# Kernel tuning notes

Hardware: AMD Instinct MI355X
Metric: run time of the kernel (lower is better)

## Reference

```python
import jax, jax.numpy as jnp
import numpy as np

N = 16384   # points (batch=1, divisible by patch_size so padding is identity)
C = 512     # channels
H = 8       # num_heads
K = 1024    # patch_size
G = 48      # voxel grid extent
EPS = 1e-5
SCALE = (C // H) ** -0.5


def setup_inputs() -> dict:
    rng = np.random.default_rng(0)
    # unique occupied voxels
    flat = rng.choice(G ** 3, size=N, replace=False)
    gx = flat // (G * G); gy = (flat // G) % G; gz = flat % G
    coords = np.stack([gx, gy, gz], 1).astype(np.int64)
    # occupancy LUT on padded grid -> neighbor index per 3x3x3 kernel offset (-1 = empty)
    lut = -np.ones(((G + 2) ** 3,), np.int64)
    def flt(c):
        return ((c[:, 0] + 1) * (G + 2) + (c[:, 1] + 1)) * (G + 2) + (c[:, 2] + 1)
    lut[flt(coords)] = np.arange(N)
    offs = np.array([[dx, dy, dz] for dx in (-1, 0, 1) for dy in (-1, 0, 1) for dz in (-1, 0, 1)], np.int64)
    nbr = np.stack([lut[flt(coords + o)] for o in offs], 1)  # [N,27]
    # Morton (z-order) serialization order
    def spread(v):
        v = v.astype(np.int64); r = np.zeros_like(v)
        for b in range(6):
            r |= ((v >> b) & 1) << (3 * b)
        return r
    code = (spread(gx) << 2) | (spread(gy) << 1) | spread(gz)
    order = np.argsort(code, kind='stable').astype(np.int32)

    key = jax.random.key(0)
    ks = jax.random.split(key, 8)
    s = 0.02
    p = lambda k, shape: jax.random.normal(k, shape, jnp.float32) * s
    return dict(
        feat=jax.random.normal(ks[0], (N, C), jnp.float32),
        neighbor_idx=jnp.asarray(nbr, jnp.int32),
        order=jnp.asarray(order, jnp.int32),
        cpe_w=p(ks[1], (27, C, C)), cpe_b=jnp.zeros((C,), jnp.float32),
        cpe_lin_w=p(ks[2], (C, C)), cpe_lin_b=jnp.zeros((C,), jnp.float32),
        cpe_ln_g=jnp.ones((C,), jnp.float32), cpe_ln_b=jnp.zeros((C,), jnp.float32),
        ln1_g=jnp.ones((C,), jnp.float32), ln1_b=jnp.zeros((C,), jnp.float32),
        qkv_w=p(ks[3], (3 * C, C)), qkv_b=jnp.zeros((3 * C,), jnp.float32),
        proj_w=p(ks[4], (C, C)), proj_b=jnp.zeros((C,), jnp.float32),
        ln2_g=jnp.ones((C,), jnp.float32), ln2_b=jnp.zeros((C,), jnp.float32),
        fc1_w=p(ks[5], (4 * C, C)), fc1_b=jnp.zeros((4 * C,), jnp.float32),
        fc2_w=p(ks[6], (C, 4 * C)), fc2_b=jnp.zeros((C,), jnp.float32),
    )


def _ln(x, g, b):
    m = x.mean(-1, keepdims=True)
    v = ((x - m) ** 2).mean(-1, keepdims=True)
    return (x - m) * jax.lax.rsqrt(v + EPS) * g + b


def _block(feat, neighbor_idx, order, cpe_w, cpe_b, cpe_lin_w, cpe_lin_b,
           cpe_ln_g, cpe_ln_b, ln1_g, ln1_b, qkv_w, qkv_b, proj_w, proj_b,
           ln2_g, ln2_b, fc1_w, fc1_b, fc2_w, fc2_b):
    # ---- CPE: SubMConv3d(3x3x3) -> Linear -> LayerNorm, residual ----
    valid = neighbor_idx >= 0
    idx = jnp.maximum(neighbor_idx, 0)
    h = jnp.zeros_like(feat)
    for kk in range(27):  # fixed kernel volume
        g = jnp.where(valid[:, kk:kk + 1], feat[idx[:, kk]], 0.0)
        h = h + g @ cpe_w[kk].T
    h = h + cpe_b
    h = h @ cpe_lin_w.T + cpe_lin_b
    h = _ln(h, cpe_ln_g, cpe_ln_b)
    feat = feat + h
    # ---- Serialized windowed attention (pre-norm, residual) ----
    x = _ln(feat, ln1_g, ln1_b)
    qkv = (x @ qkv_w.T + qkv_b)[order]                 # gather by serialized order
    qkv = qkv.reshape(N // K, K, 3, H, C // H)         # [P,K,3,H,hd]
    q = qkv[:, :, 0].transpose(0, 2, 1, 3)             # [P,H,K,hd]
    k = qkv[:, :, 1].transpose(0, 2, 1, 3)
    v = qkv[:, :, 2].transpose(0, 2, 1, 3)
    attn = jax.nn.softmax(jnp.einsum('phkd,phjd->phkj', q * SCALE, k), axis=-1)
    o = jnp.einsum('phkj,phjd->phkd', attn, v).transpose(0, 2, 1, 3).reshape(N, C)
    inverse = jnp.argsort(order)                       # scatter back
    o = o[inverse] @ proj_w.T + proj_b
    feat = feat + o
    # ---- MLP (pre-norm, residual) ----
    x = _ln(feat, ln2_g, ln2_b)
    x = jax.nn.gelu(x @ fc1_w.T + fc1_b, approximate=False)
    x = x @ fc2_w.T + fc2_b
    return feat + x


def reference(feat, neighbor_idx, order, cpe_w, cpe_b, cpe_lin_w, cpe_lin_b,
              cpe_ln_g, cpe_ln_b, ln1_g, ln1_b, qkv_w, qkv_b, proj_w, proj_b,
              ln2_g, ln2_b, fc1_w, fc1_b, fc2_w, fc2_b):
    return _block(feat, neighbor_idx, order, cpe_w, cpe_b, cpe_lin_w, cpe_lin_b,
                  cpe_ln_g, cpe_ln_b, ln1_g, ln1_b, qkv_w, qkv_b, proj_w, proj_b,
                  ln2_g, ln2_b, fc1_w, fc1_b, fc2_w, fc2_b)
```

## Files before the change

### kernel.cpp

```cpp
#include <hip/hip_runtime.h>
#include <math.h>

typedef unsigned short u16;
typedef unsigned int u32;
typedef unsigned long long u64;
typedef __attribute__((ext_vector_type(8))) short short8;
typedef __attribute__((ext_vector_type(4))) float f32x4;

#define NPTS 16384
#define MAXP 98304
#define MAXTILE 3483

__device__ __forceinline__ u16 f2bf(float f) {
  u32 u = __float_as_uint(f);
  u = (u + 0x7fffu + ((u >> 16) & 1u)) >> 16;
  return (u16)u;
}
__device__ __forceinline__ float bf2f(u16 u) {
  return __uint_as_float((u32)u << 16);
}

__device__ __forceinline__ void gl2lds16(const u16* g, u16* l) {
  __builtin_amdgcn_global_load_lds(
      (const __attribute__((address_space(1))) u32*)g,
      (__attribute__((address_space(3))) u32*)l, 16, 0, 0);
}

__device__ __forceinline__ float wredsum(float v) {
#pragma unroll
  for (int m = 1; m < 64; m <<= 1) v += __shfl_xor(v, m, 64);
  return v;
}
__device__ __forceinline__ int wredsumi(int v) {
#pragma unroll
  for (int m = 1; m < 64; m <<= 1) v += __shfl_xor(v, m, 64);
  return v;
}

__global__ void cvt_all(const float* __restrict__ w0, const float* __restrict__ w1,
                        const float* __restrict__ w2, const float* __restrict__ w3,
                        const float* __restrict__ w4, const float* __restrict__ w5,
                        u16* __restrict__ dst) {
  const int i = blockIdx.x * 256 + threadIdx.x;
  const float* s;
  int li;
  if (i < 1769472) { s = w0; li = i; }
  else if (i < 1835008) { s = w1; li = i - 1769472; }
  else if (i < 2031616) { s = w2; li = i - 1835008; }
  else if (i < 2097152) { s = w3; li = i - 2031616; }
  else if (i < 2359296) { s = w4; li = i - 2097152; }
  else { s = w5; li = i - 2359296; }
  float4 v = ((const float4*)s)[li];
  ushort4 o;
  o.x = f2bf(v.x); o.y = f2bf(v.y); o.z = f2bf(v.z); o.w = f2bf(v.w);
  ((ushort4*)dst)[i] = o;
}

__global__ void cvt_feat(const float* __restrict__ s, u16* __restrict__ d) {
  int i = blockIdx.x * 256 + threadIdx.x;
  if (i >= (NPTS + 1) * 128) return;
  ushort4 o;
  if (i < NPTS * 128) {
    float4 v = ((const float4*)s)[i];
    o.x = f2bf(v.x); o.y = f2bf(v.y); o.z = f2bf(v.z); o.w = f2bf(v.w);
  } else {
    o.x = 0; o.y = 0; o.z = 0; o.w = 0;
  }
  ((ushort4*)d)[i] = o;
}

__global__ void mkinv(const int* __restrict__ order, int* __restrict__ inv) {
  int i = blockIdx.x * 256 + threadIdx.x;
  if (i < NPTS) inv[order[i]] = i;
}

__global__ __launch_bounds__(256) void cpe_count(const int* __restrict__ nbr,
                                                 int* __restrict__ cnt) {
  __shared__ int wc[4];
  const int kk = blockIdx.x;
  int c = 0;
  for (int i = threadIdx.x; i < NPTS; i += 256)
    c += (nbr[i * 27 + kk] >= 0) ? 1 : 0;
  c = wredsumi(c);
  if ((threadIdx.x & 63) == 0) wc[threadIdx.x >> 6] = c;
  __syncthreads();
  if (threadIdx.x == 0) cnt[kk] = wc[0] + wc[1] + wc[2] + wc[3];
}

__global__ void cpe_off(const int* __restrict__ cnt, int* __restrict__ off,
                        int* __restrict__ tkk, int* __restrict__ meta) {
  if (threadIdx.x != 0 || blockIdx.x != 0) return;
  int pos = 0, t = 0;
  for (int kk = 0; kk < 27; kk++) {
    off[kk] = pos;
    int tk = (cnt[kk] + 127) >> 7;
    if (pos + tk * 128 > MAXP) tk = (MAXP - pos) >> 7;
    for (int u = 0; u < tk; u++) tkk[t + u] = kk;
    t += tk;
    pos += tk * 128;
  }
  meta[0] = t;
}

__global__ __launch_bounds__(256) void cpe_scatter(
    const int* __restrict__ nbr, const int* __restrict__ cnt,
    const int* __restrict__ off, int* __restrict__ pairj,
    int* __restrict__ pairpos) {
  __shared__ int wcnt[4];
  __shared__ int running_s;
  const int kk = blockIdx.x;
  const int tid = threadIdx.x, wave = tid >> 6, lane = tid & 63;
  const int base = off[kk];
  if (tid == 0) running_s = 0;
  __syncthreads();
  for (int c0 = 0; c0 < NPTS; c0 += 256) {
    const int i = c0 + tid;
    const int v = nbr[i * 27 + kk];
    const bool valid = v >= 0;
    const u64 m = __ballot(valid);
    if (lane == 0) wcnt[wave] = __popcll(m);
    __syncthreads();
    int woff = 0;
    for (int w = 0; w < wave; w++) woff += wcnt[w];
    const int ctot = wcnt[0] + wcnt[1] + wcnt[2] + wcnt[3];
    const int rank = running_s + woff + __popcll(m & ((1ull << lane) - 1ull));
    int pp = -1;
    if (valid) {
      const int t = base + rank;
      if (t < MAXP) { pairj[t] = v; pp = t; }
    }
    pairpos[i * 27 + kk] = pp;
    __syncthreads();
    if (tid == 0) running_s += ctot;
    __syncthreads();
  }
  const int total = cnt[kk];
  const int padded = (total + 127) & ~127;
  for (int p = total + tid; p < padded; p += 256)
    if (base + p < MAXP) pairj[base + p] = NPTS;
}

__global__ __launch_bounds__(256, 2) void gemm_pair(
    const u16* __restrict__ Abase, const u16* __restrict__ Bw,
    const int* __restrict__ meta, const int* __restrict__ tkk,
    const int* __restrict__ pairj, u16* __restrict__ outp) {
  if ((int)blockIdx.x >= meta[0]) return;
  __shared__ __align__(16) u16 sA[128 * 32];
  __shared__ __align__(16) u16 sB[128 * 32];
  const int tid = threadIdx.x;
  const int wave = tid >> 6, lane = tid & 63;
  const int quad = lane >> 4, tl = lane & 15;
  const int wr = wave >> 1, wc = wave & 1;
  const int p0 = blockIdx.x * 128, n0 = blockIdx.y * 128;
  const int kk = tkk[blockIdx.x];
  const int srow = lane >> 2, scol = lane & 3;

  int r[2]; int ca[2];
#pragma unroll
  for (int o = 0; o < 2; o++) {
    r[o] = wave * 32 + o * 16 + srow;
    const int sw = (r[o] + (r[o] >> 2)) & 3;
    ca[o] = (scol ^ sw) * 8;
  }
  const int j0 = pairj[p0 + r[0]];
  const int j1 = pairj[p0 + r[1]];
  const u16* a0 = Abase + (size_t)j0 * 512 + ca[0];
  const u16* a1 = Abase + (size_t)j1 * 512 + ca[1];
  const u16* b0 = Bw + (size_t)kk * 262144 + (size_t)(n0 + r[0]) * 512 + ca[0];
  const u16* b1 = Bw + (size_t)kk * 262144 + (size_t)(n0 + r[1]) * 512 + ca[1];
  u16* ldsA0 = &sA[(wave * 32) * 32];
  u16* ldsA1 = &sA[(wave * 32 + 16) * 32];
  u16* ldsB0 = &sB[(wave * 32) * 32];
  u16* ldsB1 = &sB[(wave * 32 + 16) * 32];

  f32x4 acc[4][4] = {};
#pragma unroll 1
  for (int kc = 0; kc < 512; kc += 32) {
    __syncthreads();
    gl2lds16(a0 + kc, ldsA0);
    gl2lds16(b0 + kc, ldsB0);
    gl2lds16(a1 + kc, ldsA1);
    gl2lds16(b1 + kc, ldsB1);
    __syncthreads();
    short8 fa[4], fb[4];
#pragma unroll
    for (int i = 0; i < 4; i++) {
      const int ra = wr * 64 + i * 16 + tl;
      fa[i] = *(const short8*)&sA[ra * 32 + ((quad ^ ((ra + (ra >> 2)) & 3)) * 8)];
      const int rb = wc * 64 + i * 16 + tl;
      fb[i] = *(const short8*)&sB[rb * 32 + ((quad ^ ((rb + (rb >> 2)) & 3)) * 8)];
    }
#pragma unroll
    for (int i = 0; i < 4; i++)
#pragma unroll
      for (int j = 0; j < 4; j++)
        acc[i][j] = __builtin_amdgcn_mfma_f32_16x16x32_bf16(fa[i], fb[j], acc[i][j], 0, 0, 0);
  }

#pragma unroll
  for (int i = 0; i < 4; i++) {
    const int pB = p0 + wr * 64 + i * 16 + quad * 4;
#pragma unroll
    for (int j = 0; j < 4; j++) {
      const int n = n0 + wc * 64 + j * 16 + tl;
      f32x4 c = acc[i][j];
#pragma unroll
      for (int rr = 0; rr < 4; rr++)
        outp[(size_t)(pB + rr) * 512 + n] = f2bf(c[rr]);
    }
  }
}

__global__ __launch_bounds__(256, 4) void cpe_reduce(
    const u16* __restrict__ outp, const int* __restrict__ pairpos,
    const float* __restrict__ bias, u16* __restrict__ h) {
  const int wave = threadIdx.x >> 6, lane = threadIdx.x & 63;
  const int i = blockIdx.x * 4 + wave;
  const int c = lane * 8;
  float acc[8];
  const float4 b0 = *(const float4*)(bias + c);
  const float4 b1 = *(const float4*)(bias + c + 4);
  acc[0] = b0.x; acc[1] = b0.y; acc[2] = b0.z; acc[3] = b0.w;
  acc[4] = b1.x; acc[5] = b1.y; acc[6] = b1.z; acc[7] = b1.w;
  const int* pp = pairpos + i * 27;
#pragma unroll 1
  for (int kk = 0; kk < 27; kk++) {
    const int pos = pp[kk];
    if (pos >= 0) {
      const u16* row = outp + (size_t)pos * 512 + c;
      ushort4 u0 = *(const ushort4*)row;
      ushort4 u1 = *(const ushort4*)(row + 4);
      acc[0] += bf2f(u0.x); acc[1] += bf2f(u0.y);
      acc[2] += bf2f(u0.z); acc[3] += bf2f(u0.w);
      acc[4] += bf2f(u1.x); acc[5] += bf2f(u1.y);
      acc[6] += bf2f(u1.z); acc[7] += bf2f(u1.w);
    }
  }
  ushort4 o0, o1;
  o0.x = f2bf(acc[0]); o0.y = f2bf(acc[1]); o0.z = f2bf(acc[2]); o0.w = f2bf(acc[3]);
  o1.x = f2bf(acc[4]); o1.y = f2bf(acc[5]); o1.z = f2bf(acc[6]); o1.w = f2bf(acc[7]);
  *(ushort4*)(h + (size_t)i * 512 + c) = o0;
  *(ushort4*)(h + (size_t)i * 512 + c + 4) = o1;
}

__global__ __launch_bounds__(256) void vtrans(const u16* __restrict__ vr,
                                              u16* __restrict__ vt) {
  __shared__ u16 t[64 * 72];
  const int bid = blockIdx.x;
  const int ph = bid >> 4, jt = bid & 15;
  const u16* src = vr + (size_t)ph * 65536 + jt * 64 * 64;
  u16* dst = vt + (size_t)ph * 65536 + jt * 64;
  const int tid = threadIdx.x;
  {
    const int j = tid >> 2, d0 = (tid & 3) * 16;
    uint4 w0 = *(const uint4*)(src + j * 64 + d0);
    uint4 w1 = *(const uint4*)(src + j * 64 + d0 + 8);
    *(uint4*)&t[j * 72 + d0] = w0;
    *(uint4*)&t[j * 72 + d0 + 8] = w1;
  }
  __syncthreads();
  {
    const int dr = tid >> 2, j0 = (tid & 3) * 16;
    u16 tmp[16];
#pragma unroll
    for (int e = 0; e < 16; e++) tmp[e] = t[(j0 + e) * 72 + dr];
    *(uint4*)(dst + (size_t)dr * 1024 + j0) = *(uint4*)&tmp[0];
    *(uint4*)(dst + (size_t)dr * 1024 + j0 + 8) = *(uint4*)&tmp[8];
  }
}

enum { EP_BF16 = 0, EP_QKV = 2, EP_RES = 3, EP_GELU = 4 };

template <int EP>
__global__ __launch_bounds__(256, 2) void gemm_nt(
    const u16* __restrict__ A, const u16* __restrict__ B, int M, int N, int K,
    const float* __restrict__ bias, float* __restrict__ outf,
    u16* __restrict__ outb, const float* __restrict__ res,
    const int* __restrict__ inv, u16* __restrict__ oq, u16* __restrict__ okk,
    u16* __restrict__ ov) {
  __shared__ __align__(16) u16 sA[128 * 32];
  __shared__ __align__(16) u16 sB[128 * 32];
  const int tid = threadIdx.x;
  const int wave = tid >> 6, lane = tid & 63;
  const int quad = lane >> 4, tl = lane & 15;
  const int wr = wave >> 1, wc = wave & 1;
  const int m0 = blockIdx.x * 128, n0 = blockIdx.y * 128;
  const int srow = lane >> 2, scol = lane & 3;

  f32x4 acc[4][4] = {};

  for (int kt = 0; kt < K; kt += 32) {
    __syncthreads();
#pragma unroll
    for (int o = 0; o < 2; o++) {
      const int r = wave * 32 + o * 16 + srow;
      const int sw = (r + (r >> 2)) & 3;
      const int ca = (scol ^ sw) * 8;
      gl2lds16(A + (size_t)(m0 + r) * K + kt + ca, &sA[(wave * 32 + o * 16) * 32]);
      gl2lds16(B + (size_t)(n0 + r) * K + kt + ca, &sB[(wave * 32 + o * 16) * 32]);
    }
    __syncthreads();
    short8 fa[4], fb[4];
#pragma unroll
    for (int i = 0; i < 4; i++) {
      const int ra = wr * 64 + i * 16 + tl;
      fa[i] = *(const short8*)&sA[ra * 32 + ((quad ^ ((ra + (ra >> 2)) & 3)) * 8)];
      const int rb = wc * 64 + i * 16 + tl;
      fb[i] = *(const short8*)&sB[rb * 32 + ((quad ^ ((rb + (rb >> 2)) & 3)) * 8)];
    }
#pragma unroll
    for (int i = 0; i < 4; i++)
#pragma unroll
      for (int j = 0; j < 4; j++)
        acc[i][j] = __builtin_amdgcn_mfma_f32_16x16x32_bf16(fa[i], fb[j], acc[i][j], 0, 0, 0);
  }

#pragma unroll
  for (int i = 0; i < 4; i++) {
    const int mB = m0 + wr * 64 + i * 16 + quad * 4;
#pragma unroll
    for (int j = 0; j < 4; j++) {
      const int n = n0 + wc * 64 + j * 16 + tl;
      const float bv = bias[n];
      f32x4 c = acc[i][j];
#pragma unroll
      for (int r = 0; r < 4; r++) {
        const int m = mB + r;
        float v = c[r] + bv;
        if (EP == EP_BF16) {
          outb[(size_t)m * N + n] = f2bf(v);
        } else if (EP == EP_RES) {
          outf[(size_t)m * N + n] = v + res[(size_t)m * N + n];
        } else if (EP == EP_GELU) {
          float g = 0.5f * v * (1.0f + erff(v * 0.70710678118654752f));
          outb[(size_t)m * N + n] = f2bf(g);
        } else if (EP == EP_QKV) {
          const int s = n >> 9, hh = (n >> 6) & 7, d = n & 63;
          const int pos = inv[m];
          const size_t base = (size_t)((pos >> 10) * 8 + hh) * 65536;
          const int jj = pos & 1023;
          if (s == 0) oq[base + (size_t)jj * 64 + d] = f2bf(v * 0.125f);
          else if (s == 1) okk[base + (size_t)jj * 64 + d] = f2bf(v);
          else ov[base + (size_t)jj * 64 + d] = f2bf(v);
        }
      }
    }
  }
}

__global__ __launch_bounds__(256, 2) void attn(
    const u16* __restrict__ qs, const u16* __restrict__ kk_s,
    const u16* __restrict__ vts, const int* __restrict__ order,
    u16* __restrict__ obf) {
  __shared__ __align__(16) u16 Qt[128 * 64];
  __shared__ __align__(16) u16 Kt[64 * 64];
  __shared__ __align__(16) u16 Vt[64 * 64];
  __shared__ __align__(16) u16 Pl[4][32 * 72];
  const int tid = threadIdx.x;
  const int wave = tid >> 6, lane = tid & 63;
  const int quad = lane >> 4, tl = lane & 15;
  const int bid = blockIdx.x;
  const int p = bid >> 6, h = (bid >> 3) & 7, qt = bid & 7;
  const size_t base = (size_t)(p * 8 + h) * 65536;

  {
    const u16* Qg = qs + base + qt * 8192;
#pragma unroll
    for (int i = 0; i < 4; i++) {
      const int op = wave * 4 + i;
      const int r = op * 8 + (lane >> 3);
      const int c8 = ((lane & 7) ^ (r & 7)) * 8;
      gl2lds16(Qg + r * 64 + c8, &Qt[op * 512]);
    }
  }

  float ls[2][4] = {};
  f32x4 acco[2][4] = {};

  for (int kt = 0; kt < 16; kt++) {
    __syncthreads();
    const u16* Kg = kk_s + base + kt * 4096;
    const u16* Vg = vts + base + kt * 64;
#pragma unroll
    for (int i = 0; i < 2; i++) {
      const int op = wave * 2 + i;
      const int r = op * 8 + (lane >> 3);
      const int c8 = ((lane & 7) ^ (r & 7)) * 8;
      gl2lds16(Kg + r * 64 + c8, &Kt[op * 512]);
      gl2lds16(Vg + r * 1024 + c8, &Vt[op * 512]);
    }
    __syncthreads();

    f32x4 accs[2][4] = {};
#pragma unroll
    for (int kd = 0; kd < 2; kd++) {
      short8 qa[2], kb[4];
#pragma unroll
      for (int a = 0; a < 2; a++) {
        const int r = wave * 32 + a * 16 + tl;
        const int oct = (kd * 4 + quad) ^ (r & 7);
        qa[a] = *(const short8*)&Qt[r * 64 + oct * 8];
      }
#pragma unroll
      for (int b = 0; b < 4; b++) {
        const int r = b * 16 + tl;
        const int oct = (kd * 4 + quad) ^ (r & 7);
        kb[b] = *(const short8*)&Kt[r * 64 + oct * 8];
      }
#pragma unroll
      for (int a = 0; a < 2; a++)
#pragma unroll
        for (int b = 0; b < 4; b++)
          accs[a][b] = __builtin_amdgcn_mfma_f32_16x16x32_bf16(qa[a], kb[b], accs[a][b], 0, 0, 0);
    }

    u16* plw = &Pl[wave][0];
#pragma unroll
    for (int a = 0; a < 2; a++)
#pragma unroll
      for (int c = 0; c < 4; c++) {
#pragma unroll
        for (int r = 0; r < 4; r++) {
          const float pe = __expf(accs[a][c][r]);
          accs[a][c][r] = pe;
          ls[a][r] += pe;
          plw[(a * 16 + quad * 4 + r) * 72 + c * 16 + tl] = f2bf(pe);
        }
      }

#pragma unroll
    for (int k2 = 0; k2 < 2; k2++) {
      short8 pa[2], vb[4];
#pragma unroll
      for (int a = 0; a < 2; a++)
        pa[a] = *(const short8*)&plw[(a * 16 + tl) * 72 + k2 * 32 + quad * 8];
#pragma unroll
      for (int b = 0; b < 4; b++) {
        const int rb = b * 16 + tl;
        vb[b] = *(const short8*)&Vt[rb * 64 + (((k2 * 4 + quad) ^ (rb & 7)) * 8)];
      }
#pragma unroll
      for (int a = 0; a < 2; a++)
#pragma unroll
        for (int b = 0; b < 4; b++)
          acco[a][b] = __builtin_amdgcn_mfma_f32_16x16x32_bf16(pa[a], vb[b], acco[a][b], 0, 0, 0);
    }
  }

#pragma unroll
  for (int a = 0; a < 2; a++)
#pragma unroll
    for (int r = 0; r < 4; r++) {
#pragma unroll
      for (int mk = 1; mk < 16; mk <<= 1) ls[a][r] += __shfl_xor(ls[a][r], mk, 64);
    }

  const int q0 = p * 1024 + qt * 128 + wave * 32;
#pragma unroll
  for (int a = 0; a < 2; a++)
#pragma unroll
    for (int r = 0; r < 4; r++) {
      const int orig = order[q0 + a * 16 + quad * 4 + r];
      const float il = 1.0f / ls[a][r];
#pragma unroll
      for (int b = 0; b < 4; b++)
        obf[(size_t)orig * 512 + h * 64 + b * 16 + tl] = f2bf(acco[a][b][r] * il);
    }
}

__global__ __launch_bounds__(256, 4) void ln_fuse1(
    const u16* __restrict__ h2, const float* __restrict__ feat,
    const float* __restrict__ cg, const float* __restrict__ cb,
    const float* __restrict__ g1, const float* __restrict__ b1,
    float* __restrict__ feat1, u16* __restrict__ xbf) {
  const int wave = threadIdx.x >> 6, lane = threadIdx.x & 63;
  const size_t row = (size_t)blockIdx.x * 4 + wave;
  const int c0 = lane * 4, c1 = 256 + lane * 4;
  const u16* hr = h2 + row * 512;
  ushort4 ha = *(const ushort4*)(hr + c0);
  ushort4 hb = *(const ushort4*)(hr + c1);
  float h[8];
  h[0] = bf2f(ha.x); h[1] = bf2f(ha.y); h[2] = bf2f(ha.z); h[3] = bf2f(ha.w);
  h[4] = bf2f(hb.x); h[5] = bf2f(hb.y); h[6] = bf2f(hb.z); h[7] = bf2f(hb.w);
  float s = 0.0f, q = 0.0f;
#pragma unroll
  for (int i = 0; i < 8; i++) { s += h[i]; q += h[i] * h[i]; }
  s = wredsum(s); q = wredsum(q);
  const float mean = s * (1.0f / 512.0f);
  const float var = q * (1.0f / 512.0f) - mean * mean;
  const float rs = rsqrtf(var + 1e-5f);
  float4 ga = *(const float4*)(cg + c0), gb = *(const float4*)(cg + c1);
  float4 ba = *(const float4*)(cb + c0), bb = *(const float4*)(cb + c1);
  const float* fr = feat + row * 512;
  float4 fa = *(const float4*)(fr + c0), fb = *(const float4*)(fr + c1);
  float f[8];
  f[0] = fa.x + (h[0] - mean) * rs * ga.x + ba.x;
  f[1] = fa.y + (h[1] - mean) * rs * ga.y + ba.y;
  f[2] = fa.z + (h[2] - mean) * rs * ga.z + ba.z;
  f[3] = fa.w + (h[3] - mean) * rs * ga.w + ba.w;
  f[4] = fb.x + (h[4] - mean) * rs * gb.x + bb.x;
  f[5] = fb.y + (h[5] - mean) * rs * gb.y + bb.y;
  f[6] = fb.z + (h[6] - mean) * rs * gb.z + bb.z;
  f[7] = fb.w + (h[7] - mean) * rs * gb.w + bb.w;
  float* f1r = feat1 + row * 512;
  *(float4*)(f1r + c0) = make_float4(f[0], f[1], f[2], f[3]);
  *(float4*)(f1r + c1) = make_float4(f[4], f[5], f[6], f[7]);
  float s2 = 0.0f, q2 = 0.0f;
#pragma unroll
  for (int i = 0; i < 8; i++) { s2 += f[i]; q2 += f[i] * f[i]; }
  s2 = wredsum(s2); q2 = wredsum(q2);
  const float mean2 = s2 * (1.0f / 512.0f);
  const float var2 = q2 * (1.0f / 512.0f) - mean2 * mean2;
  const float rs2 = rsqrtf(var2 + 1e-5f);
  float4 g1a = *(const float4*)(g1 + c0), g1b = *(const float4*)(g1 + c1);
  float4 b1a = *(const float4*)(b1 + c0), b1b = *(const float4*)(b1 + c1);
  ushort4 o0, o1;
  o0.x = f2bf((f[0] - mean2) * rs2 * g1a.x + b1a.x);
  o0.y = f2bf((f[1] - mean2) * rs2 * g1a.y + b1a.y);
  o0.z = f2bf((f[2] - mean2) * rs2 * g1a.z + b1a.z);
  o0.w = f2bf((f[3] - mean2) * rs2 * g1a.w + b1a.w);
  o1.x = f2bf((f[4] - mean2) * rs2 * g1b.x + b1b.x);
  o1.y = f2bf((f[5] - mean2) * rs2 * g1b.y + b1b.y);
  o1.z = f2bf((f[6] - mean2) * rs2 * g1b.z + b1b.z);
  o1.w = f2bf((f[7] - mean2) * rs2 * g1b.w + b1b.w);
  *(ushort4*)(xbf + row * 512 + c0) = o0;
  *(ushort4*)(xbf + row * 512 + c1) = o1;
}

__global__ __launch_bounds__(256, 4) void ln_only(
    const float* __restrict__ x, const float* __restrict__ g,
    const float* __restrict__ b_, u16* __restrict__ o) {
  const int wave = threadIdx.x >> 6, lane = threadIdx.x & 63;
  const size_t row = (size_t)blockIdx.x * 4 + wave;
  const int c0 = lane * 4, c1 = 256 + lane * 4;
  const float* xr = x + row * 512;
  float4 a = *(const float4*)(xr + c0);
  float4 b = *(const float4*)(xr + c1);
  float s = a.x + a.y + a.z + a.w + b.x + b.y + b.z + b.w;
  float q = a.x * a.x + a.y * a.y + a.z * a.z + a.w * a.w +
            b.x * b.x + b.y * b.y + b.z * b.z + b.w * b.w;
  s = wredsum(s); q = wredsum(q);
  const float mean = s * (1.0f / 512.0f);
  const float var = q * (1.0f / 512.0f) - mean * mean;
  const float rs = rsqrtf(var + 1e-5f);
  float4 ga = *(const float4*)(g + c0), gb = *(const float4*)(g + c1);
  float4 ba = *(const float4*)(b_ + c0), bb = *(const float4*)(b_ + c1);
  ushort4 o0, o1;
  o0.x = f2bf((a.x - mean) * rs * ga.x + ba.x);
  o0.y = f2bf((a.y - mean) * rs * ga.y + ba.y);
  o0.z = f2bf((a.z - mean) * rs * ga.z + ba.z);
  o0.w = f2bf((a.w - mean) * rs * ga.w + ba.w);
  o1.x = f2bf((b.x - mean) * rs * gb.x + bb.x);
  o1.y = f2bf((b.y - mean) * rs * gb.y + bb.y);
  o1.z = f2bf((b.z - mean) * rs * gb.z + bb.z);
  o1.w = f2bf((b.w - mean) * rs * gb.w + bb.w);
  *(ushort4*)(o + row * 512 + c0) = o0;
  *(ushort4*)(o + row * 512 + c1) = o1;
}

extern "C" void kernel_launch(void* const* d_in, const int* in_sizes, int n_in,
                              void* d_out, int out_size, void* d_ws, size_t ws_size,
                              hipStream_t stream) {
  (void)in_sizes; (void)n_in; (void)out_size; (void)ws_size;
  const float* feat = (const float*)d_in[0];
  const int* nbr = (const int*)d_in[1];
  const int* order = (const int*)d_in[2];
  const float* cpe_w = (const float*)d_in[3];
  const float* cpe_b = (const float*)d_in[4];
  const float* cpe_lin_w = (const float*)d_in[5];
  const float* cpe_lin_b = (const float*)d_in[6];
  const float* cpe_ln_g = (const float*)d_in[7];
  const float* cpe_ln_b = (const float*)d_in[8];
  const float* ln1_g = (const float*)d_in[9];
  const float* ln1_b = (const float*)d_in[10];
  const float* qkv_w = (const float*)d_in[11];
  const float* qkv_b = (const float*)d_in[12];
  const float* proj_w = (const float*)d_in[13];
  const float* proj_b = (const float*)d_in[14];
  const float* ln2_g = (const float*)d_in[15];
  const float* ln2_b = (const float*)d_in[16];
  const float* fc1_w = (const float*)d_in[17];
  const float* fc1_b = (const float*)d_in[18];
  const float* fc2_w = (const float*)d_in[19];
  const float* fc2_b = (const float*)d_in[20];
  float* out = (float*)d_out;

  char* ws = (char*)d_ws;
  size_t off = 0;
  auto alloc = [&](size_t bytes) {
    char* p = ws + off;
    off += (bytes + 255) & ~(size_t)255;
    return p;
  };
  u16* featbf = (u16*)alloc((size_t)(NPTS + 1) * 512 * 2);
  u16* w_cpe = (u16*)alloc((size_t)27 * 512 * 512 * 2);
  u16* w_cl = (u16*)alloc((size_t)512 * 512 * 2);
  u16* w_qkv = (u16*)alloc((size_t)1536 * 512 * 2);
  u16* w_proj = (u16*)alloc((size_t)512 * 512 * 2);
  u16* w_fc1 = (u16*)alloc((size_t)2048 * 512 * 2);
  u16* w_fc2 = (u16*)alloc((size_t)512 * 2048 * 2);
  u16* hbf = (u16*)alloc((size_t)NPTS * 512 * 2);
  char* big = alloc((size_t)NPTS * 2048 * 2);
  float* feat1 = (float*)alloc((size_t)NPTS * 512 * 4);
  int* inv = (int*)alloc((size_t)NPTS * 4);
  int* cnt = (int*)alloc(27 * 4);
  int* offs = (int*)alloc(27 * 4);
  int* meta = (int*)alloc(256);
  int* tkk = (int*)alloc((size_t)(MAXTILE + 1) * 4);
  int* pairj = (int*)alloc((size_t)MAXP * 4);
  int* pairpos = (int*)alloc((size_t)NPTS * 27 * 4);

  u16* out_pair = (u16*)big;
  u16* h2 = (u16*)big;
  u16* qsb = (u16*)big;
  u16* ksb = qsb + (size_t)NPTS * 512;
  u16* vrow = ksb + (size_t)NPTS * 512;
  u16* vtb = vrow + (size_t)NPTS * 512;
  u16* tbf = (u16*)big;
  u16* xbf = hbf;
  u16* obf = hbf;
  u16* x2bf = featbf;

  cvt_feat<<<dim3(((NPTS + 1) * 128 + 255) / 256), dim3(256), 0, stream>>>(feat, featbf);
  cvt_all<<<dim3(10240), dim3(256), 0, stream>>>(cpe_w, cpe_lin_w, qkv_w, proj_w,
                                                 fc1_w, fc2_w, w_cpe);
  mkinv<<<dim3(NPTS / 256), dim3(256), 0, stream>>>(order, inv);

  cpe_count<<<dim3(27), dim3(256), 0, stream>>>(nbr, cnt);
  cpe_off<<<dim3(1), dim3(64), 0, stream>>>(cnt, offs, tkk, meta);
  cpe_scatter<<<dim3(27), dim3(256), 0, stream>>>(nbr, cnt, offs, pairj, pairpos);
  gemm_pair<<<dim3(MAXTILE, 4), dim3(256), 0, stream>>>(featbf, w_cpe, meta, tkk,
                                                        pairj, out_pair);
  cpe_reduce<<<dim3(NPTS / 4), dim3(256), 0, stream>>>(out_pair, pairpos, cpe_b, hbf);

  gemm_nt<EP_BF16><<<dim3(128, 4), dim3(256), 0, stream>>>(
      hbf, w_cl, NPTS, 512, 512, cpe_lin_b, nullptr, h2, nullptr, nullptr,
      nullptr, nullptr, nullptr);
  ln_fuse1<<<dim3(NPTS / 4), dim3(256), 0, stream>>>(
      h2, feat, cpe_ln_g, cpe_ln_b, ln1_g, ln1_b, feat1, xbf);
  gemm_nt<EP_QKV><<<dim3(128, 12), dim3(256), 0, stream>>>(
      xbf, w_qkv, NPTS, 1536, 512, qkv_b, nullptr, nullptr, nullptr, inv,
      qsb, ksb, vrow);
  vtrans<<<dim3(2048), dim3(256), 0, stream>>>(vrow, vtb);
  attn<<<dim3(1024), dim3(256), 0, stream>>>(qsb, ksb, vtb, order, obf);
  gemm_nt<EP_RES><<<dim3(128, 4), dim3(256), 0, stream>>>(
      obf, w_proj, NPTS, 512, 512, proj_b, out, nullptr, feat1, nullptr,
      nullptr, nullptr, nullptr);
  ln_only<<<dim3(NPTS / 4), dim3(256), 0, stream>>>(out, ln2_g, ln2_b, x2bf);
  gemm_nt<EP_GELU><<<dim3(128, 16), dim3(256), 0, stream>>>(
      x2bf, w_fc1, NPTS, 2048, 512, fc1_b, nullptr, tbf, nullptr, nullptr,
      nullptr, nullptr, nullptr);
  gemm_nt<EP_RES><<<dim3(128, 4), dim3(256), 0, stream>>>(
      tbf, w_fc2, NPTS, 512, 2048, fc2_b, out, nullptr, out, nullptr,
      nullptr, nullptr, nullptr);
}
```

Measured before the change: 603.7 us.

## Parallelize CPE pair planning, merge conversions, split-K fc2, shrink pair grid

The per-offset count and scatter kernels ran only 27 blocks with serial loops and barriers. They are replaced by a per-wave ballot count, a single planning kernel that builds prefix offsets, and a wide scatter kernel. The feature and weight bf16 conversions are merged into one launch. The pair-GEMM grid is transposed and bounded at the real tile maximum, so far fewer blocks launch only to exit. The fc2 GEMM is split along K into two halves that write bf16 partials, followed by a reduction kernel that adds bias and the residual. This raises occupancy for the K=2048 GEMM, but the bf16 partials slightly reduce accuracy and the extra pass adds memory traffic.

```diff
diff --git a/kernel.cpp b/kernel.cpp
--- a/kernel.cpp
+++ b/kernel.cpp
@@ -9,7 +9,7 @@
 
 #define NPTS 16384
 #define MAXP 98304
-#define MAXTILE 3483
+#define MAXTILE 768
 
 __device__ __forceinline__ u16 f2bf(float f) {
   u32 u = __float_as_uint(f);
@@ -31,42 +31,36 @@
   for (int m = 1; m < 64; m <<= 1) v += __shfl_xor(v, m, 64);
   return v;
 }
-__device__ __forceinline__ int wredsumi(int v) {
-#pragma unroll
-  for (int m = 1; m < 64; m <<= 1) v += __shfl_xor(v, m, 64);
-  return v;
-}
-
-__global__ void cvt_all(const float* __restrict__ w0, const float* __restrict__ w1,
-                        const float* __restrict__ w2, const float* __restrict__ w3,
-                        const float* __restrict__ w4, const float* __restrict__ w5,
-                        u16* __restrict__ dst) {
+
+__global__ void cvt_comb(const float* __restrict__ feat,
+                         const float* __restrict__ w0, const float* __restrict__ w1,
+                         const float* __restrict__ w2, const float* __restrict__ w3,
+                         const float* __restrict__ w4, const float* __restrict__ w5,
+                         u16* __restrict__ dst) {
   const int i = blockIdx.x * 256 + threadIdx.x;
-  const float* s;
-  int li;
-  if (i < 1769472) { s = w0; li = i; }
-  else if (i < 1835008) { s = w1; li = i - 1769472; }
-  else if (i < 2031616) { s = w2; li = i - 1835008; }
-  else if (i < 2097152) { s = w3; li = i - 2031616; }
-  else if (i < 2359296) { s = w4; li = i - 2097152; }
-  else { s = w5; li = i - 2359296; }
-  float4 v = ((const float4*)s)[li];
+  if (i >= 4718720) return;
   ushort4 o;
-  o.x = f2bf(v.x); o.y = f2bf(v.y); o.z = f2bf(v.z); o.w = f2bf(v.w);
+  if (i < 2097280) {
+    if (i < 2097152) {
+      float4 v = ((const float4*)feat)[i];
+      o.x = f2bf(v.x); o.y = f2bf(v.y); o.z = f2bf(v.z); o.w = f2bf(v.w);
+    } else {
+      o.x = 0; o.y = 0; o.z = 0; o.w = 0;
+    }
+  } else {
+    const int j = i - 2097280;
+    const float* s;
+    int li;
+    if (j < 1769472) { s = w0; li = j; }
+    else if (j < 1835008) { s = w1; li = j - 1769472; }
+    else if (j < 2031616) { s = w2; li = j - 1835008; }
+    else if (j < 2097152) { s = w3; li = j - 2031616; }
+    else if (j < 2359296) { s = w4; li = j - 2097152; }
+    else { s = w5; li = j - 2359296; }
+    float4 v = ((const float4*)s)[li];
+    o.x = f2bf(v.x); o.y = f2bf(v.y); o.z = f2bf(v.z); o.w = f2bf(v.w);
+  }
   ((ushort4*)dst)[i] = o;
-}
-
-__global__ void cvt_feat(const float* __restrict__ s, u16* __restrict__ d) {
-  int i = blockIdx.x * 256 + threadIdx.x;
-  if (i >= (NPTS + 1) * 128) return;
-  ushort4 o;
-  if (i < NPTS * 128) {
-    float4 v = ((const float4*)s)[i];
-    o.x = f2bf(v.x); o.y = f2bf(v.y); o.z = f2bf(v.z); o.w = f2bf(v.w);
-  } else {
-    o.x = 0; o.y = 0; o.z = 0; o.w = 0;
-  }
-  ((ushort4*)d)[i] = o;
 }
 
 __global__ void mkinv(const int* __restrict__ order, int* __restrict__ inv) {
@@ -74,85 +68,96 @@
   if (i < NPTS) inv[order[i]] = i;
 }
 
-__global__ __launch_bounds__(256) void cpe_count(const int* __restrict__ nbr,
-                                                 int* __restrict__ cnt) {
-  __shared__ int wc[4];
-  const int kk = blockIdx.x;
-  int c = 0;
-  for (int i = threadIdx.x; i < NPTS; i += 256)
-    c += (nbr[i * 27 + kk] >= 0) ? 1 : 0;
-  c = wredsumi(c);
-  if ((threadIdx.x & 63) == 0) wc[threadIdx.x >> 6] = c;
+__global__ __launch_bounds__(256) void cpe_cnt(const int* __restrict__ nbr,
+                                               int* __restrict__ wcnt) {
+  const int wglob = blockIdx.x * 4 + (threadIdx.x >> 6);
+  const int lane = threadIdx.x & 63;
+  const int i = wglob * 64 + lane;
+  const int* row = nbr + i * 27;
+#pragma unroll 1
+  for (int kk = 0; kk < 27; kk++) {
+    const u64 m = __ballot(row[kk] >= 0);
+    if (lane == 0) wcnt[wglob * 27 + kk] = (int)__popcll(m);
+  }
+}
+
+__global__ __launch_bounds__(256) void cpe_plan(
+    const int* __restrict__ wcnt, int* __restrict__ chunkoff,
+    int* __restrict__ off, int* __restrict__ tkk, int* __restrict__ meta,
+    int* __restrict__ pairj) {
+  __shared__ int s_cnt[27], s_off[27], s_ts[27], s_tk[27];
+  const int tid = threadIdx.x;
+  if (tid < 27) {
+    int run = 0;
+#pragma unroll 1
+    for (int c = 0; c < 256; c++) {
+      chunkoff[c * 27 + tid] = run;
+      run += wcnt[c * 27 + tid];
+    }
+    s_cnt[tid] = run;
+  }
   __syncthreads();
-  if (threadIdx.x == 0) cnt[kk] = wc[0] + wc[1] + wc[2] + wc[3];
-}
-
-__global__ void cpe_off(const int* __restrict__ cnt, int* __restrict__ off,
-                        int* __restrict__ tkk, int* __restrict__ meta) {
-  if (threadIdx.x != 0 || blockIdx.x != 0) return;
-  int pos = 0, t = 0;
+  if (tid == 0) {
+    int pos = 0, t = 0;
+#pragma unroll 1
+    for (int kk = 0; kk < 27; kk++) {
+      s_off[kk] = pos;
+      off[kk] = pos;
+      int tk = (s_cnt[kk] + 127) >> 7;
+      if (pos + tk * 128 > MAXP) tk = (MAXP - pos) >> 7;
+      s_ts[kk] = t;
+      s_tk[kk] = tk;
+      t += tk;
+      pos += tk * 128;
+    }
+    meta[0] = t;
+  }
+  __syncthreads();
+#pragma unroll 1
   for (int kk = 0; kk < 27; kk++) {
-    off[kk] = pos;
-    int tk = (cnt[kk] + 127) >> 7;
-    if (pos + tk * 128 > MAXP) tk = (MAXP - pos) >> 7;
-    for (int u = 0; u < tk; u++) tkk[t + u] = kk;
-    t += tk;
-    pos += tk * 128;
-  }
-  meta[0] = t;
-}
-
-__global__ __launch_bounds__(256) void cpe_scatter(
-    const int* __restrict__ nbr, const int* __restrict__ cnt,
+    const int ts = s_ts[kk], tk = s_tk[kk];
+    for (int u = tid; u < tk; u += 256) tkk[ts + u] = kk;
+    const int base = s_off[kk], total = s_cnt[kk], padded = tk * 128;
+    for (int p2 = total + tid; p2 < padded; p2 += 256) pairj[base + p2] = NPTS;
+  }
+}
+
+__global__ __launch_bounds__(256) void cpe_scat(
+    const int* __restrict__ nbr, const int* __restrict__ chunkoff,
     const int* __restrict__ off, int* __restrict__ pairj,
     int* __restrict__ pairpos) {
-  __shared__ int wcnt[4];
-  __shared__ int running_s;
-  const int kk = blockIdx.x;
-  const int tid = threadIdx.x, wave = tid >> 6, lane = tid & 63;
-  const int base = off[kk];
-  if (tid == 0) running_s = 0;
-  __syncthreads();
-  for (int c0 = 0; c0 < NPTS; c0 += 256) {
-    const int i = c0 + tid;
-    const int v = nbr[i * 27 + kk];
+  const int wglob = blockIdx.x * 4 + (threadIdx.x >> 6);
+  const int lane = threadIdx.x & 63;
+  const int i = wglob * 64 + lane;
+  const int* row = nbr + i * 27;
+  const u64 below = (1ull << lane) - 1ull;
+#pragma unroll 1
+  for (int kk = 0; kk < 27; kk++) {
+    const int v = row[kk];
     const bool valid = v >= 0;
     const u64 m = __ballot(valid);
-    if (lane == 0) wcnt[wave] = __popcll(m);
-    __syncthreads();
-    int woff = 0;
-    for (int w = 0; w < wave; w++) woff += wcnt[w];
-    const int ctot = wcnt[0] + wcnt[1] + wcnt[2] + wcnt[3];
-    const int rank = running_s + woff + __popcll(m & ((1ull << lane) - 1ull));
     int pp = -1;
     if (valid) {
-      const int t = base + rank;
+      const int t = off[kk] + chunkoff[wglob * 27 + kk] + (int)__popcll(m & below);
       if (t < MAXP) { pairj[t] = v; pp = t; }
     }
     pairpos[i * 27 + kk] = pp;
-    __syncthreads();
-    if (tid == 0) running_s += ctot;
-    __syncthreads();
-  }
-  const int total = cnt[kk];
-  const int padded = (total + 127) & ~127;
-  for (int p = total + tid; p < padded; p += 256)
-    if (base + p < MAXP) pairj[base + p] = NPTS;
+  }
 }
 
 __global__ __launch_bounds__(256, 2) void gemm_pair(
     const u16* __restrict__ Abase, const u16* __restrict__ Bw,
     const int* __restrict__ meta, const int* __restrict__ tkk,
     const int* __restrict__ pairj, u16* __restrict__ outp) {
-  if ((int)blockIdx.x >= meta[0]) return;
+  if ((int)blockIdx.y >= meta[0]) return;
   __shared__ __align__(16) u16 sA[128 * 32];
   __shared__ __align__(16) u16 sB[128 * 32];
   const int tid = threadIdx.x;
   const int wave = tid >> 6, lane = tid & 63;
   const int quad = lane >> 4, tl = lane & 15;
   const int wr = wave >> 1, wc = wave & 1;
-  const int p0 = blockIdx.x * 128, n0 = blockIdx.y * 128;
-  const int kk = tkk[blockIdx.x];
+  const int p0 = blockIdx.y * 128, n0 = blockIdx.x * 128;
+  const int kk = tkk[blockIdx.y];
   const int srow = lane >> 2, scol = lane & 3;
 
   int r[2]; int ca[2];
@@ -346,6 +351,73 @@
       }
     }
   }
+}
+
+__global__ __launch_bounds__(256, 2) void gemm_fc2(
+    const u16* __restrict__ A, const u16* __restrict__ B, u16* __restrict__ part) {
+  __shared__ __align__(16) u16 sA[128 * 32];
+  __shared__ __align__(16) u16 sB[128 * 32];
+  const int tid = threadIdx.x;
+  const int wave = tid >> 6, lane = tid & 63;
+  const int quad = lane >> 4, tl = lane & 15;
+  const int wr = wave >> 1, wc = wave & 1;
+  const int m0 = blockIdx.x * 128, n0 = blockIdx.y * 128;
+  const int kb = blockIdx.z * 1024;
+  const int srow = lane >> 2, scol = lane & 3;
+
+  f32x4 acc[4][4] = {};
+  for (int kt = kb; kt < kb + 1024; kt += 32) {
+    __syncthreads();
+#pragma unroll
+    for (int o = 0; o < 2; o++) {
+      const int r = wave * 32 + o * 16 + srow;
+      const int sw = (r + (r >> 2)) & 3;
+      const int ca = (scol ^ sw) * 8;
+      gl2lds16(A + (size_t)(m0 + r) * 2048 + kt + ca, &sA[(wave * 32 + o * 16) * 32]);
+      gl2lds16(B + (size_t)(n0 + r) * 2048 + kt + ca, &sB[(wave * 32 + o * 16) * 32]);
+    }
+    __syncthreads();
+    short8 fa[4], fb[4];
+#pragma unroll
+    for (int i = 0; i < 4; i++) {
+      const int ra = wr * 64 + i * 16 + tl;
+      fa[i] = *(const short8*)&sA[ra * 32 + ((quad ^ ((ra + (ra >> 2)) & 3)) * 8)];
+      const int rb = wc * 64 + i * 16 + tl;
+      fb[i] = *(const short8*)&sB[rb * 32 + ((quad ^ ((rb + (rb >> 2)) & 3)) * 8)];
+    }
+#pragma unroll
+    for (int i = 0; i < 4; i++)
+#pragma unroll
+      for (int j = 0; j < 4; j++)
+        acc[i][j] = __builtin_amdgcn_mfma_f32_16x16x32_bf16(fa[i], fb[j], acc[i][j], 0, 0, 0);
+  }
+  u16* pz = part + (size_t)blockIdx.z * NPTS * 512;
+#pragma unroll
+  for (int i = 0; i < 4; i++) {
+    const int mB = m0 + wr * 64 + i * 16 + quad * 4;
+#pragma unroll
+    for (int j = 0; j < 4; j++) {
+      const int n = n0 + wc * 64 + j * 16 + tl;
+      f32x4 c = acc[i][j];
+#pragma unroll
+      for (int rr = 0; rr < 4; rr++)
+        pz[(size_t)(mB + rr) * 512 + n] = f2bf(c[rr]);
+    }
+  }
+}
+
+__global__ void fc2_red(const u16* __restrict__ part, const float* __restrict__ bias,
+                        float* __restrict__ out) {
+  const int i = blockIdx.x * 256 + threadIdx.x;
+  const ushort4 a = ((const ushort4*)part)[i];
+  const ushort4 b = ((const ushort4*)part)[i + 2097152];
+  const float4 bb = ((const float4*)bias)[i & 127];
+  float4 o = ((const float4*)out)[i];
+  o.x += bf2f(a.x) + bf2f(b.x) + bb.x;
+  o.y += bf2f(a.y) + bf2f(b.y) + bb.y;
+  o.z += bf2f(a.z) + bf2f(b.z) + bb.z;
+  o.w += bf2f(a.w) + bf2f(b.w) + bb.w;
+  ((float4*)out)[i] = o;
 }
 
 __global__ __launch_bounds__(256, 2) void attn(
@@ -603,12 +675,13 @@
   char* big = alloc((size_t)NPTS * 2048 * 2);
   float* feat1 = (float*)alloc((size_t)NPTS * 512 * 4);
   int* inv = (int*)alloc((size_t)NPTS * 4);
-  int* cnt = (int*)alloc(27 * 4);
   int* offs = (int*)alloc(27 * 4);
   int* meta = (int*)alloc(256);
   int* tkk = (int*)alloc((size_t)(MAXTILE + 1) * 4);
   int* pairj = (int*)alloc((size_t)MAXP * 4);
   int* pairpos = (int*)alloc((size_t)NPTS * 27 * 4);
+  int* wcnt = (int*)alloc((size_t)256 * 27 * 4);
+  int* chunkoff = (int*)alloc((size_t)256 * 27 * 4);
 
   u16* out_pair = (u16*)big;
   u16* h2 = (u16*)big;
@@ -617,19 +690,19 @@
   u16* vrow = ksb + (size_t)NPTS * 512;
   u16* vtb = vrow + (size_t)NPTS * 512;
   u16* tbf = (u16*)big;
+  u16* fc2p = (u16*)feat1;
   u16* xbf = hbf;
   u16* obf = hbf;
   u16* x2bf = featbf;
 
-  cvt_feat<<<dim3(((NPTS + 1) * 128 + 255) / 256), dim3(256), 0, stream>>>(feat, featbf);
-  cvt_all<<<dim3(10240), dim3(256), 0, stream>>>(cpe_w, cpe_lin_w, qkv_w, proj_w,
-                                                 fc1_w, fc2_w, w_cpe);
+  cvt_comb<<<dim3(18433), dim3(256), 0, stream>>>(feat, cpe_w, cpe_lin_w, qkv_w,
+                                                  proj_w, fc1_w, fc2_w, featbf);
   mkinv<<<dim3(NPTS / 256), dim3(256), 0, stream>>>(order, inv);
 
-  cpe_count<<<dim3(27), dim3(256), 0, stream>>>(nbr, cnt);
-  cpe_off<<<dim3(1), dim3(64), 0, stream>>>(cnt, offs, tkk, meta);
-  cpe_scatter<<<dim3(27), dim3(256), 0, stream>>>(nbr, cnt, offs, pairj, pairpos);
-  gemm_pair<<<dim3(MAXTILE, 4), dim3(256), 0, stream>>>(featbf, w_cpe, meta, tkk,
+  cpe_cnt<<<dim3(64), dim3(256), 0, stream>>>(nbr, wcnt);
+  cpe_plan<<<dim3(1), dim3(256), 0, stream>>>(wcnt, chunkoff, offs, tkk, meta, pairj);
+  cpe_scat<<<dim3(64), dim3(256), 0, stream>>>(nbr, chunkoff, offs, pairj, pairpos);
+  gemm_pair<<<dim3(4, MAXTILE), dim3(256), 0, stream>>>(featbf, w_cpe, meta, tkk,
                                                         pairj, out_pair);
   cpe_reduce<<<dim3(NPTS / 4), dim3(256), 0, stream>>>(out_pair, pairpos, cpe_b, hbf);
 
@@ -650,7 +723,6 @@
   gemm_nt<EP_GELU><<<dim3(128, 16), dim3(256), 0, stream>>>(
       x2bf, w_fc1, NPTS, 2048, 512, fc1_b, nullptr, tbf, nullptr, nullptr,
       nullptr, nullptr, nullptr);
-  gemm_nt<EP_RES><<<dim3(128, 4), dim3(256), 0, stream>>>(
-      tbf, w_fc2, NPTS, 512, 2048, fc2_b, out, nullptr, out, nullptr,
-      nullptr, nullptr, nullptr);
-}
+  gemm_fc2<<<dim3(128, 4, 2), dim3(256), 0, stream>>>(tbf, w_fc2, fc2p);
+  fc2_red<<<dim3(8192), dim3(256), 0, stream>>>(fc2p, fc2_b, out);
+}
```

Measured after the change: 617.9 us. 1.02x slower.
